# Kernel optimization log

Measured on AMD Instinct MI355X. Metric: run time of the kernel, lower is better.

The kernel has to match this reference:

```python
import jax, jax.numpy as jnp
import numpy as np

LATENT = 1024

def setup_inputs() -> dict:
    key = jax.random.key(0)
    ks = jax.random.split(key, 8)
    N, BD, H, W = 1024, 2048, 7, 7
    C = 64  # num classes (pos == orient, required by stack dim=2)
    feat = jax.random.normal(ks[0], (N, BD, H, W), dtype=jnp.float32)
    fc1_w = jax.random.normal(ks[1], (LATENT, BD), dtype=jnp.float32) * (2.0 / BD) ** 0.5
    fc1_b = jnp.zeros((LATENT,), dtype=jnp.float32)
    cls_pos_w = jax.random.normal(ks[2], (C, LATENT), dtype=jnp.float32) * (2.0 / LATENT) ** 0.5
    cls_pos_b = jnp.zeros((C,), dtype=jnp.float32)
    cls_orient_w = jax.random.normal(ks[3], (C, LATENT), dtype=jnp.float32) * (2.0 / LATENT) ** 0.5
    cls_orient_b = jnp.zeros((C,), dtype=jnp.float32)
    reg_pos_w = jax.random.normal(ks[4], (C, 3, LATENT), dtype=jnp.float32) * (2.0 / LATENT) ** 0.5
    reg_pos_b = jnp.zeros((C, 3), dtype=jnp.float32)
    reg_orient_w = jax.random.normal(ks[5], (C, 4, LATENT), dtype=jnp.float32) * (2.0 / LATENT) ** 0.5
    reg_orient_b = jnp.zeros((C, 4), dtype=jnp.float32)
    return {"feat": feat, "fc1_w": fc1_w, "fc1_b": fc1_b,
            "cls_pos_w": cls_pos_w, "cls_pos_b": cls_pos_b,
            "cls_orient_w": cls_orient_w, "cls_orient_b": cls_orient_b,
            "reg_pos_w": reg_pos_w, "reg_pos_b": reg_pos_b,
            "reg_orient_w": reg_orient_w, "reg_orient_b": reg_orient_b}

def _to_label(pred):
    # relu(sum(cumprod(pred > 0.5, dim=1)) - 1) -> int64 ordinal label
    run = jnp.cumprod((pred > 0.5).astype(jnp.int32), axis=1)
    return jnp.maximum(run.sum(axis=1) - 1, 0).astype(jnp.int32)

def reference(feat, fc1_w, fc1_b, cls_pos_w, cls_pos_b, cls_orient_w, cls_orient_b,
              reg_pos_w, reg_pos_b, reg_orient_w, reg_orient_b):
    # AdaptiveAvgPool2d(1) + flatten -> [N, backbone_dim]
    x = feat.mean(axis=(2, 3))
    # fc1 + ReLU (dropout is identity at inference)
    x = jax.nn.relu(x @ fc1_w.T + fc1_b)  # [N, latent]
    cls_x = jax.nn.sigmoid(x @ cls_pos_w.T + cls_pos_b)      # [N, C]
    cls_q = jax.nn.sigmoid(x @ cls_orient_w.T + cls_orient_b)  # [N, C]
    idx_x = _to_label(cls_x)
    idx_q = _to_label(cls_q)
    # Hard-routed expert heads: gather per-sample expert weights, batched matvec
    p_x = jnp.einsum('nkd,nd->nk', reg_pos_w[idx_x], x) + reg_pos_b[idx_x]        # [N, 3]
    p_q = jnp.einsum('nkd,nd->nk', reg_orient_w[idx_q], x) + reg_orient_b[idx_q]  # [N, 4]
    pose = jnp.concatenate([p_x, p_q], axis=1)       # [N, 7]
    pose_cls = jnp.stack([cls_x, cls_q], axis=2)     # [N, C, 2]
    return pose, pose_cls
```

## Files before the change

### kernel.cpp

```cpp
#include <hip/hip_runtime.h>
#include <hip/hip_bf16.h>

#define N_SAMP   1024
#define BD       2048
#define LATENT_D 1024
#define NCLS     64
#define HW       49

typedef __attribute__((ext_vector_type(8))) _Float16 f16x8;
typedef __attribute__((ext_vector_type(4))) float f32x4;
typedef unsigned short u16;

__device__ __forceinline__ size_t split_idx_r(int row, int k, int rows) {
    const int kg = k >> 5, ke = k & 31;
    const int c2 = (ke * 2) ^ (((row >> 1) & 3) << 4);
    return ((size_t)(kg * rows + row) * 32) + (c2 >> 1);
}

__device__ __forceinline__ void split2(float v, u16* p0, u16* p1, size_t idx) {
    _Float16 h0 = (_Float16)v;
    _Float16 h1 = (_Float16)(v - (float)h0);
    p0[idx] = *(u16*)&h0;
    p1[idx] = *(u16*)&h1;
}

__global__ __launch_bounds__(256) void pool_kernel(const float* __restrict__ feat,
                                                   u16* __restrict__ a0,
                                                   u16* __restrict__ a1) {
    __shared__ float buf[256 * HW];
    const int b = blockIdx.x;
    const float4* src = reinterpret_cast<const float4*>(feat + (size_t)b * (256 * HW));
    float4* dst = reinterpret_cast<float4*>(buf);
    #pragma unroll
    for (int i = threadIdx.x; i < (256 * HW) / 4; i += 256) dst[i] = src[i];
    __syncthreads();
    const float* p = buf + threadIdx.x * HW;
    float s = 0.f;
    #pragma unroll
    for (int k = 0; k < HW; ++k) s += p[k];
    const float v = s * (1.0f / 49.0f);
    const int n = b >> 3;
    const int d = (b & 7) * 256 + threadIdx.x;
    split2(v, a0, a1, split_idx_r(n, d, N_SAMP));
}

__global__ __launch_bounds__(256) void wsplit_kernel(const float* __restrict__ W,
                                                     const float* __restrict__ Wp,
                                                     const float* __restrict__ Wo,
                                                     u16* __restrict__ b0,
                                                     u16* __restrict__ b1,
                                                     u16* __restrict__ c0,
                                                     u16* __restrict__ c1) {
    const int b = blockIdx.x;
    if (b < 8192) {
        const int row = b >> 3;
        const int d = (b & 7) * 256 + threadIdx.x;
        split2(W[(size_t)row * BD + d], b0, b1, split_idx_r(row, d, LATENT_D));
    } else {
        const int b2 = b - 8192;
        const int row = b2 >> 2;
        const int d = (b2 & 3) * 256 + threadIdx.x;
        const float v = row < 64 ? Wp[(size_t)row * LATENT_D + d]
                                 : Wo[(size_t)(row - 64) * LATENT_D + d];
        split2(v, c0, c1, split_idx_r(row, d, 128));
    }
}

#define GLL16(g, l) __builtin_amdgcn_global_load_lds( \
    (const __attribute__((address_space(1))) void*)(g), \
    (__attribute__((address_space(3))) void*)(l), 16, 0, 0)

__global__ __launch_bounds__(256, 2) void split_mfma(
    const u16* __restrict__ A0, const u16* __restrict__ A1,
    const u16* __restrict__ B0, const u16* __restrict__ B1,
    float* __restrict__ part, int ksteps, int rowsA, int rowsB, int ldc) {
    __shared__ u16 lds[2][4 * 4096];
    const int bn = blockIdx.x, bm = blockIdx.y, kz = blockIdx.z;
    const int tid = threadIdx.x, lane = tid & 63, wv = tid >> 6;
    const int wrow = (wv >> 1) * 64, wcol = (wv & 1) * 64;
    const int r15 = lane & 15, khi = lane >> 4;

    const u16* gA[2] = {A0, A1};
    const u16* gB[2] = {B0, B1};
    const int kg0 = kz * ksteps;

    auto stage = [&](int kg, int buf) {
        #pragma unroll
        for (int s = 0; s < 2; ++s) {
            const u16* g = gA[s] + ((size_t)(kg * rowsA + bm * 128 + wv * 32) * 32) + lane * 8;
            u16* l = &lds[buf][s * 4096 + wv * 1024 + lane * 8];
            GLL16(g, l);
            GLL16(g + 512, l + 512);
        }
        #pragma unroll
        for (int s = 0; s < 2; ++s) {
            const u16* g = gB[s] + ((size_t)(kg * rowsB + bn * 128 + wv * 32) * 32) + lane * 8;
            u16* l = &lds[buf][(2 + s) * 4096 + wv * 1024 + lane * 8];
            GLL16(g, l);
            GLL16(g + 512, l + 512);
        }
    };

    f32x4 acc[4][4];
    #pragma unroll
    for (int i = 0; i < 4; ++i)
        #pragma unroll
        for (int j = 0; j < 4; ++j) acc[i][j] = (f32x4){0.f, 0.f, 0.f, 0.f};

    stage(kg0, 0);
    asm volatile("s_waitcnt vmcnt(0)" ::: "memory");
    __builtin_amdgcn_s_barrier();

    int cur = 0;
    for (int ks = 0; ks < ksteps; ++ks) {
        f16x8 af[4][2], bf[4][2];
        #pragma unroll
        for (int i = 0; i < 4; ++i) {
            const int rowA = wrow + i * 16 + r15;
            const int offA = rowA * 64 + ((khi * 16) ^ (((rowA >> 1) & 3) << 4));
            const int rowB = wcol + i * 16 + r15;
            const int offB = rowB * 64 + ((khi * 16) ^ (((rowB >> 1) & 3) << 4));
            #pragma unroll
            for (int s = 0; s < 2; ++s) {
                af[i][s] = *(const f16x8*)((const char*)&lds[cur][s * 4096] + offA);
                bf[i][s] = *(const f16x8*)((const char*)&lds[cur][(2 + s) * 4096] + offB);
            }
        }
        if (ks + 1 < ksteps) stage(kg0 + ks + 1, cur ^ 1);
        #pragma unroll
        for (int p = 0; p < 4; ++p) {
            const int pa = p >> 1, pb = p & 1;
            #pragma unroll
            for (int i = 0; i < 4; ++i)
                #pragma unroll
                for (int j = 0; j < 4; ++j)
                    acc[i][j] = __builtin_amdgcn_mfma_f32_16x16x32_f16(
                        af[i][pa], bf[j][pb], acc[i][j], 0, 0, 0);
        }
        asm volatile("s_waitcnt vmcnt(0)" ::: "memory");
        __builtin_amdgcn_s_barrier();
        cur ^= 1;
    }

    float* pt = part + (size_t)kz * ((size_t)N_SAMP * ldc);
    #pragma unroll
    for (int i = 0; i < 4; ++i) {
        const int row0 = bm * 128 + wrow + i * 16 + khi * 4;
        #pragma unroll
        for (int j = 0; j < 4; ++j) {
            const int col = bn * 128 + wcol + j * 16 + r15;
            #pragma unroll
            for (int q = 0; q < 4; ++q)
                pt[(size_t)(row0 + q) * ldc + col] = acc[i][j][q];
        }
    }
}

__global__ __launch_bounds__(256) void reduce_fc1(const float* __restrict__ part,
                                                  const float* __restrict__ bias,
                                                  float* __restrict__ x,
                                                  u16* __restrict__ x0,
                                                  u16* __restrict__ x1,
                                                  int nsplit) {
    const int i = blockIdx.x * 256 + threadIdx.x;
    const float4* p = reinterpret_cast<const float4*>(part);
    float4 s = p[i];
    for (int z = 1; z < nsplit; ++z) {
        const float4 t = p[(size_t)z * 262144 + i];
        s.x += t.x; s.y += t.y; s.z += t.z; s.w += t.w;
    }
    const float4 b = reinterpret_cast<const float4*>(bias)[i & 255];
    s.x = fmaxf(s.x + b.x, 0.f); s.y = fmaxf(s.y + b.y, 0.f);
    s.z = fmaxf(s.z + b.z, 0.f); s.w = fmaxf(s.w + b.w, 0.f);
    reinterpret_cast<float4*>(x)[i] = s;
    const int n = i >> 8, d0 = (i & 255) * 4;
    split2(s.x, x0, x1, split_idx_r(n, d0 + 0, N_SAMP));
    split2(s.y, x0, x1, split_idx_r(n, d0 + 1, N_SAMP));
    split2(s.z, x0, x1, split_idx_r(n, d0 + 2, N_SAMP));
    split2(s.w, x0, x1, split_idx_r(n, d0 + 3, N_SAMP));
}

__global__ __launch_bounds__(128) void decode_expert(const float* __restrict__ part2,
                                                     const float* __restrict__ bp,
                                                     const float* __restrict__ bo,
                                                     const float* __restrict__ x,
                                                     const float* __restrict__ wpos,
                                                     const float* __restrict__ bpos,
                                                     const float* __restrict__ wori,
                                                     const float* __restrict__ bori,
                                                     float* __restrict__ pose_cls,
                                                     float* __restrict__ pose,
                                                     int nsplit) {
    const int n = blockIdx.x, t = threadIdx.x;
    __shared__ float xs[LATENT_D];
    __shared__ int esh[2];

    const float4* x4 = reinterpret_cast<const float4*>(x + (size_t)n * LATENT_D);
    float4* xs4 = reinterpret_cast<float4*>(xs);
    xs4[t] = x4[t];
    xs4[t + 128] = x4[t + 128];

    float s = (t < 64) ? bp[t] : bo[t - 64];
    for (int z = 0; z < nsplit; ++z)
        s += part2[(size_t)z * (N_SAMP * 128) + (size_t)n * 128 + t];
    const float sig = 1.0f / (1.0f + expf(-s));
    const int head = t >> 6, c = t & 63;
    pose_cls[(size_t)n * (NCLS * 2) + c * 2 + head] = sig;

    const unsigned long long mask = __ballot(s > 0.0f);
    if (c == 0) {
        const unsigned long long inv = ~mask;
        const int run = inv ? __builtin_ctzll(inv) : 64;
        const int lab = run - 1;
        esh[head] = lab > 0 ? lab : 0;
    }
    __syncthreads();

    const int e = esh[head];
    const int nk = head ? 4 : 3;
    for (int kk = 0; kk < nk; ++kk) {
        const float* wr = head ? wori + (size_t)(e * 4 + kk) * LATENT_D
                               : wpos + (size_t)(e * 3 + kk) * LATENT_D;
        const float bb = head ? bori[e * 4 + kk] : bpos[e * 3 + kk];
        const float4* w4 = reinterpret_cast<const float4*>(wr);
        float s2 = 0.f;
        #pragma unroll
        for (int i = 0; i < 4; ++i) {
            const int q = c + i * 64;
            const float4 a = w4[q];
            s2 += a.x * xs[q * 4] + a.y * xs[q * 4 + 1] + a.z * xs[q * 4 + 2] + a.w * xs[q * 4 + 3];
        }
        #pragma unroll
        for (int off = 32; off > 0; off >>= 1) s2 += __shfl_down(s2, off);
        if (c == 0) pose[(size_t)n * 7 + (head ? 3 + kk : kk)] = s2 + bb;
    }
}

extern "C" void kernel_launch(void* const* d_in, const int* in_sizes, int n_in,
                              void* d_out, int out_size, void* d_ws, size_t ws_size,
                              hipStream_t stream) {
    const float* feat   = (const float*)d_in[0];
    const float* fc1_w  = (const float*)d_in[1];
    const float* fc1_b  = (const float*)d_in[2];
    const float* cpw    = (const float*)d_in[3];
    const float* cpb    = (const float*)d_in[4];
    const float* cow    = (const float*)d_in[5];
    const float* cob    = (const float*)d_in[6];
    const float* rpw    = (const float*)d_in[7];
    const float* rpb    = (const float*)d_in[8];
    const float* row_   = (const float*)d_in[9];
    const float* rob    = (const float*)d_in[10];

    float* out = (float*)d_out;
    float* pose     = out;
    float* pose_cls = out + (size_t)N_SAMP * 7;

    char* ws = (char*)d_ws;
    const size_t MB = (size_t)1 << 20;
    size_t off = 0;
    auto take = [&](size_t bytes) { char* p = ws + off; off += (bytes + 255) & ~(size_t)255; return p; };

    u16* A0 = (u16*)take(4 * MB);
    u16* A1 = (u16*)take(4 * MB);
    u16* B0 = (u16*)take(4 * MB);
    u16* B1 = (u16*)take(4 * MB);
    u16* C0 = (u16*)take(256 * 1024);
    u16* C1 = (u16*)take(256 * 1024);
    u16* X0 = (u16*)take(2 * MB);
    u16* X1 = (u16*)take(2 * MB);
    float* x = (float*)take(4 * MB);

    int nsplit = 8;
    while (nsplit > 1 && off + (size_t)nsplit * 4 * MB + 5 * MB > ws_size) nsplit >>= 1;
    float* part = (float*)take((size_t)nsplit * 4 * MB);
    int nsplit_c = 8;
    while (nsplit_c > 1 && off + (size_t)nsplit_c * 512 * 1024 > ws_size) nsplit_c >>= 1;
    float* part2 = (float*)take((size_t)nsplit_c * 512 * 1024);

    wsplit_kernel<<<8704, 256, 0, stream>>>(fc1_w, cpw, cow, B0, B1, C0, C1);
    pool_kernel<<<(N_SAMP * BD) / 256, 256, 0, stream>>>(feat, A0, A1);
    split_mfma<<<dim3(8, 8, nsplit), 256, 0, stream>>>(
        A0, A1, B0, B1, part, 64 / nsplit, N_SAMP, LATENT_D, LATENT_D);
    reduce_fc1<<<1024, 256, 0, stream>>>(part, fc1_b, x, X0, X1, nsplit);
    split_mfma<<<dim3(1, 8, nsplit_c), 256, 0, stream>>>(
        X0, X1, C0, C1, part2, 32 / nsplit_c, N_SAMP, 128, 128);
    decode_expert<<<N_SAMP, 128, 0, stream>>>(part2, cpb, cob, x, rpw, rpb, row_, rob,
                                              pose_cls, pose, nsplit_c);
}
```

Baseline: 154.4 us.

## Fuse pooling and weight split into one prep kernel with direct LDS loads

Merges the weight fp16-split kernel and the average-pool kernel into a single launch, so pooling and weight conversion blocks can run concurrently. The feature tile is now loaded with global_load_lds (direct-to-LDS) instead of float4 register round-trips. The class-head split-K factor is reduced from 8 to 4 and the workspace fallback margin is loosened. Each block still uses the full pool LDS allocation even for weight-split blocks, which can limit occupancy for those blocks.

```diff
diff --git a/kernel.cpp b/kernel.cpp
--- a/kernel.cpp
+++ b/kernel.cpp
@@ -24,51 +24,52 @@
     p1[idx] = *(u16*)&h1;
 }
 
-__global__ __launch_bounds__(256) void pool_kernel(const float* __restrict__ feat,
+#define GLL16(g, l) __builtin_amdgcn_global_load_lds( \
+    (const __attribute__((address_space(1))) void*)(g), \
+    (__attribute__((address_space(3))) void*)(l), 16, 0, 0)
+
+__global__ __launch_bounds__(256) void prep_kernel(const float* __restrict__ feat,
+                                                   const float* __restrict__ W,
+                                                   const float* __restrict__ Wp,
+                                                   const float* __restrict__ Wo,
                                                    u16* __restrict__ a0,
-                                                   u16* __restrict__ a1) {
+                                                   u16* __restrict__ a1,
+                                                   u16* __restrict__ b0,
+                                                   u16* __restrict__ b1,
+                                                   u16* __restrict__ c0,
+                                                   u16* __restrict__ c1) {
     __shared__ float buf[256 * HW];
     const int b = blockIdx.x;
-    const float4* src = reinterpret_cast<const float4*>(feat + (size_t)b * (256 * HW));
-    float4* dst = reinterpret_cast<float4*>(buf);
-    #pragma unroll
-    for (int i = threadIdx.x; i < (256 * HW) / 4; i += 256) dst[i] = src[i];
-    __syncthreads();
-    const float* p = buf + threadIdx.x * HW;
-    float s = 0.f;
-    #pragma unroll
-    for (int k = 0; k < HW; ++k) s += p[k];
-    const float v = s * (1.0f / 49.0f);
-    const int n = b >> 3;
-    const int d = (b & 7) * 256 + threadIdx.x;
-    split2(v, a0, a1, split_idx_r(n, d, N_SAMP));
-}
-
-__global__ __launch_bounds__(256) void wsplit_kernel(const float* __restrict__ W,
-                                                     const float* __restrict__ Wp,
-                                                     const float* __restrict__ Wo,
-                                                     u16* __restrict__ b0,
-                                                     u16* __restrict__ b1,
-                                                     u16* __restrict__ c0,
-                                                     u16* __restrict__ c1) {
-    const int b = blockIdx.x;
+    const int tid = threadIdx.x;
     if (b < 8192) {
-        const int row = b >> 3;
-        const int d = (b & 7) * 256 + threadIdx.x;
+        const int lane = tid & 63, wv = tid >> 6;
+        const float* src = feat + (size_t)b * (256 * HW);
+        for (int c = wv; c < 49; c += 4)
+            GLL16(src + c * 256 + lane * 4, (char*)buf + c * 1024 + lane * 16);
+        asm volatile("s_waitcnt vmcnt(0)" ::: "memory");
+        __syncthreads();
+        const float* p = buf + tid * HW;
+        float s = 0.f;
+        #pragma unroll
+        for (int k = 0; k < HW; ++k) s += p[k];
+        const float v = s * (1.0f / 49.0f);
+        const int n = b >> 3;
+        const int d = (b & 7) * 256 + tid;
+        split2(v, a0, a1, split_idx_r(n, d, N_SAMP));
+    } else if (b < 16384) {
+        const int b2 = b - 8192;
+        const int row = b2 >> 3;
+        const int d = (b2 & 7) * 256 + tid;
         split2(W[(size_t)row * BD + d], b0, b1, split_idx_r(row, d, LATENT_D));
     } else {
-        const int b2 = b - 8192;
+        const int b2 = b - 16384;
         const int row = b2 >> 2;
-        const int d = (b2 & 3) * 256 + threadIdx.x;
+        const int d = (b2 & 3) * 256 + tid;
         const float v = row < 64 ? Wp[(size_t)row * LATENT_D + d]
                                  : Wo[(size_t)(row - 64) * LATENT_D + d];
         split2(v, c0, c1, split_idx_r(row, d, 128));
     }
 }
-
-#define GLL16(g, l) __builtin_amdgcn_global_load_lds( \
-    (const __attribute__((address_space(1))) void*)(g), \
-    (__attribute__((address_space(3))) void*)(l), 16, 0, 0)
 
 __global__ __launch_bounds__(256, 2) void split_mfma(
     const u16* __restrict__ A0, const u16* __restrict__ A1,
@@ -271,14 +272,14 @@
     float* x = (float*)take(4 * MB);
 
     int nsplit = 8;
-    while (nsplit > 1 && off + (size_t)nsplit * 4 * MB + 5 * MB > ws_size) nsplit >>= 1;
+    while (nsplit > 1 && off + (size_t)nsplit * 4 * MB + 3 * MB > ws_size) nsplit >>= 1;
     float* part = (float*)take((size_t)nsplit * 4 * MB);
-    int nsplit_c = 8;
+    int nsplit_c = 4;
     while (nsplit_c > 1 && off + (size_t)nsplit_c * 512 * 1024 > ws_size) nsplit_c >>= 1;
     float* part2 = (float*)take((size_t)nsplit_c * 512 * 1024);
 
-    wsplit_kernel<<<8704, 256, 0, stream>>>(fc1_w, cpw, cow, B0, B1, C0, C1);
-    pool_kernel<<<(N_SAMP * BD) / 256, 256, 0, stream>>>(feat, A0, A1);
+    prep_kernel<<<16896, 256, 0, stream>>>(feat, fc1_w, cpw, cow,
+                                           A0, A1, B0, B1, C0, C1);
     split_mfma<<<dim3(8, 8, nsplit), 256, 0, stream>>>(
         A0, A1, B0, B1, part, 64 / nsplit, N_SAMP, LATENT_D, LATENT_D);
     reduce_fc1<<<1024, 256, 0, stream>>>(part, fc1_b, x, X0, X1, nsplit);
```

After: 136.2 us. 1.13x faster.
